# Performance work log

Hardware: AMD Instinct MI355X
Metric: run time of the kernel (lower is better)

## Reference

```python
import jax, jax.numpy as jnp
import numpy as np

N_EMBED = 1024
CUTOFFS = [20000, 60000, 180000]
N_VOCAB = 267735
BOUNDS = [0] + CUTOFFS + [N_VOCAB]            # cluster boundaries
N_EMBEDS = [1024, 256, 64, 16]                # n_embed / 4**i
N_TOK = 1024
N_CLUSTERS = len(CUTOFFS)                      # 3 tail clusters


def setup_inputs() -> dict:
    key = jax.random.key(0)
    ks = jax.random.split(key, 12)

    def w(k, shape):
        fan_in = shape[0]
        return (jax.random.normal(k, shape, jnp.float32) / np.sqrt(fan_in)).astype(jnp.float32)

    inp = {}
    inp["hidden"] = jax.random.normal(ks[0], (N_TOK, N_EMBED), jnp.float32)
    inp["target"] = jax.random.randint(ks[1], (N_TOK,), 0, N_VOCAB)
    # head: layers[0] = Linear(n_embed, cutoffs[0]); clusters = Linear(n_embed, n_clusters)
    inp["W_head"] = w(ks[2], (N_EMBED, BOUNDS[1]))
    inp["b_head"] = jnp.zeros((BOUNDS[1],), jnp.float32)
    inp["W_cluster"] = w(ks[3], (N_EMBED, N_CLUSTERS))
    inp["b_cluster"] = jnp.zeros((N_CLUSTERS,), jnp.float32)
    # tails: projections[i-1] = Linear(n_embed, n_embeds[i], bias=False); layers[i] = Linear(n_embeds[i], end-start)
    for i in range(1, N_CLUSTERS + 1):
        size = BOUNDS[i + 1] - BOUNDS[i]
        inp[f"W_proj{i}"] = w(ks[3 + 2 * i], (N_EMBED, N_EMBEDS[i]))
        inp[f"W_tail{i}"] = w(ks[4 + 2 * i], (N_EMBEDS[i], size))
        inp[f"b_tail{i}"] = jnp.zeros((size,), jnp.float32)
    return inp


def _adaptive_nll(hidden, target, W_head, b_head, W_cluster, b_cluster, tails):
    # head logits = [vocab cluster 0 | cluster logits], then log_softmax (matches torch.cat + log_softmax)
    head_logit = jnp.concatenate(
        [hidden @ W_head + b_head, hidden @ W_cluster + b_cluster], axis=1)  # [N, cut0 + n_clusters]
    head_lp = jax.nn.log_softmax(head_logit, axis=1)

    # cluster 0: logprob = head_lp[n, target]
    t0 = jnp.clip(target, 0, BOUNDS[1] - 1)
    lp0 = jnp.take_along_axis(head_lp, t0[:, None], axis=1)[:, 0]
    nll = jnp.where(target < BOUNDS[1], -lp0, jnp.zeros((), head_lp.dtype))

    # tail clusters i=1..3: logprob = head_lp[:, -i] + tail_log_softmax[n, target-start]
    for i, (Wp, Wt, bt) in enumerate(tails, start=1):
        start, end = BOUNDS[i], BOUNDS[i + 1]
        tail_lp = jax.nn.log_softmax((hidden @ Wp) @ Wt + bt, axis=1)  # [N, end-start]
        rel = jnp.clip(target - start, 0, end - start - 1)
        lp_i = head_lp[:, -i] + jnp.take_along_axis(tail_lp, rel[:, None], axis=1)[:, 0]
        in_bucket = (target >= start) & (target < end)
        nll = jnp.where(in_bucket, -lp_i, nll)
    return nll  # [N], per-token negative log-likelihood (keep_order=True semantics)


def reference(hidden, target, W_head, b_head, W_cluster, b_cluster,
              W_proj1, W_tail1, b_tail1,
              W_proj2, W_tail2, b_tail2,
              W_proj3, W_tail3, b_tail3):
    tails = [(W_proj1, W_tail1, b_tail1),
             (W_proj2, W_tail2, b_tail2),
             (W_proj3, W_tail3, b_tail3)]
    return _adaptive_nll(hidden, target, W_head, b_head, W_cluster, b_cluster, tails)
```

## Files before the change

### kernel.cpp

```cpp
#include <hip/hip_runtime.h>
#include <cstdint>
#include <cstddef>


typedef unsigned short u16;
typedef __attribute__((ext_vector_type(8))) __bf16 bf16x8;
typedef __attribute__((ext_vector_type(8))) u16 u16x8;
typedef __attribute__((ext_vector_type(4))) float f32x4;

#define AS1 __attribute__((address_space(1)))
#define AS3 __attribute__((address_space(3)))

struct MS { float m, s; };

__device__ __forceinline__ u16 f2bf(float f){
  union { float f; unsigned u; } v; v.f = f;
  unsigned r = v.u + 0x7fffu + ((v.u >> 16) & 1u);
  return (u16)(r >> 16);
}
__device__ __forceinline__ float bf2f(u16 x){
  union { unsigned u; float f; } v; v.u = ((unsigned)x) << 16;
  return v.f;
}
__device__ __forceinline__ void glds16(const void* g, void* l){
  __builtin_amdgcn_global_load_lds((AS1 unsigned*)(uintptr_t)g,
                                   (AS3 unsigned*)(unsigned)(uintptr_t)l, 16, 0, 0);
}

__global__ void k_cvt_hidden(const float* __restrict__ h, u16* __restrict__ a0,
                             int* __restrict__ cnt, int* __restrict__ trel){
  int g = blockIdx.x * 256 + threadIdx.x;
  if (g < 4096) trel[g] = -1;
  if (g < 4) cnt[g] = 0;
  int i = g * 8;
  f32x4 v0 = *(const f32x4*)(h + i);
  f32x4 v1 = *(const f32x4*)(h + i + 4);
  u16x8 o;
  o[0]=f2bf(v0.x); o[1]=f2bf(v0.y); o[2]=f2bf(v0.z); o[3]=f2bf(v0.w);
  o[4]=f2bf(v1.x); o[5]=f2bf(v1.y); o[6]=f2bf(v1.z); o[7]=f2bf(v1.w);
  *(u16x8*)(a0 + i) = o;
}

__global__ void k_compact(const int* __restrict__ tgt, int* __restrict__ cnt,
                          int* __restrict__ idx1, int* __restrict__ idx2,
                          int* __restrict__ idx3, int* __restrict__ pos,
                          int* __restrict__ tr0, int* __restrict__ tr1,
                          int* __restrict__ tr2, int* __restrict__ tr3){
  int n = blockIdx.x * 256 + threadIdx.x;
  int t = tgt[n];
  int p = 0;
  tr0[n] = (t < 20000) ? t : -1;
  if (t >= 20000){
    int b = (t < 60000) ? 0 : (t < 180000 ? 1 : 2);
    p = atomicAdd(&cnt[b], 1);
    if (b == 0){ idx1[p] = n; tr1[p] = t - 20000; }
    else if (b == 1){ idx2[p] = n; tr2[p] = t - 60000; }
    else { idx3[p] = n; tr3[p] = t - 180000; }
  }
  pos[n] = p;
}

__global__ void k_gather(const int* __restrict__ cnt,
                         const int* __restrict__ idx1, const int* __restrict__ idx2,
                         const int* __restrict__ idx3,
                         const u16* __restrict__ A1, const u16* __restrict__ A2,
                         const u16* __restrict__ A3,
                         u16* __restrict__ A1c, u16* __restrict__ A2c,
                         u16* __restrict__ A3c){
  int u = blockIdx.x * 256 + threadIdx.x;
  const u16* src; u16* dst;
  if (u < 32768){
    int r = u >> 5, c = u & 31;
    if (r >= cnt[0]) return;
    src = A1 + (size_t)idx1[r] * 256 + c * 8;
    dst = A1c + (size_t)r * 256 + c * 8;
  } else if (u < 40960){
    int v = u - 32768; int r = v >> 3, c = v & 7;
    if (r >= cnt[1]) return;
    src = A2 + (size_t)idx2[r] * 64 + c * 8;
    dst = A2c + (size_t)r * 64 + c * 8;
  } else {
    int v = u - 40960; int r = v >> 2, c = v & 3;
    if (r >= cnt[2]) return;
    src = A3 + (size_t)idx3[r] * 32 + c * 8;
    dst = A3c + (size_t)r * 32 + c * 8;
  }
  *(u16x8*)dst = *(const u16x8*)src;
}

struct TJob { const float* W; u16* BT; int K, N, Kpad, nrows, nx, base; };
struct TJobs { TJob j[8]; int nj; };

__global__ void k_transpose_multi(TJobs jobs){
  int id = blockIdx.x;
  int ji = 0;
  #pragma unroll
  for (int i = 1; i < 8; ++i)
    if (i < jobs.nj && id >= jobs.j[i].base) ji = i;
  TJob jb = jobs.j[ji];
  int local = id - jb.base;
  int bx = local % jb.nx;
  int by = local / jb.nx;

  __shared__ float t[64][65];
  const int n0 = bx * 64;
  const int k0 = by * 64;
  const bool al = (jb.N & 3) == 0;
  for (int i = threadIdx.x; i < 64*16; i += 256){
    int r = i >> 4, c4 = (i & 15) * 4;
    int k = k0 + r, n = n0 + c4;
    f32x4 v; v.x=0.f; v.y=0.f; v.z=0.f; v.w=0.f;
    if (k < jb.K){
      if (al && n + 3 < jb.N) v = *(const f32x4*)(jb.W + (size_t)k * jb.N + n);
      else { for (int q = 0; q < 4; ++q) if (n + q < jb.N) v[q] = jb.W[(size_t)k * jb.N + n + q]; }
    }
    t[r][c4] = v.x; t[r][c4+1] = v.y; t[r][c4+2] = v.z; t[r][c4+3] = v.w;
  }
  __syncthreads();
  for (int i = threadIdx.x; i < 64*8; i += 256){
    int rn = i >> 3, c8 = (i & 7) * 8;
    if (k0 + c8 < jb.Kpad && (n0 + rn) < jb.nrows){
      u16x8 o;
      #pragma unroll
      for (int q = 0; q < 8; ++q) o[q] = f2bf(t[c8 + q][rn]);
      *(u16x8*)(jb.BT + (size_t)(n0 + rn) * jb.Kpad + k0 + c8) = o;
    }
  }
}

__global__ __launch_bounds__(512)
void k_proj_gemm(const u16* __restrict__ A, const u16* __restrict__ BT,
                 const float* __restrict__ bc,
                 u16* __restrict__ A1, u16* __restrict__ A2,
                 u16* __restrict__ A3, float* __restrict__ cl)
{
  constexpr int BK = 64, K = 1024;
  __shared__ u16 As[256 * BK];
  __shared__ u16 Bs[128 * BK];
  const int tid  = threadIdx.x;
  const int lane = tid & 63, wid = tid >> 6;
  const int wm = wid & 3, wn = wid >> 2;
  const int l15 = lane & 15, l4 = lane >> 4;
  const int m0 = blockIdx.y * 256;
  const int n0 = blockIdx.x * 128;

  f32x4 acc[4][4];
  #pragma unroll
  for (int m = 0; m < 4; ++m)
    #pragma unroll
    for (int n = 0; n < 4; ++n){ acc[m][n].x=0.f; acc[m][n].y=0.f; acc[m][n].z=0.f; acc[m][n].w=0.f; }

  for (int kt = 0; kt < K / BK; ++kt){
    #pragma unroll
    for (int i = 0; i < 4; ++i){
      int c = wid * 4 + i;
      int row = c * 8 + lane / 8, kb = lane % 8;
      glds16((const char*)(A + (size_t)(m0 + row) * K + kt * BK) + kb * 16,
             (char*)As + c * 1024);
    }
    #pragma unroll
    for (int i = 0; i < 2; ++i){
      int c = wid * 2 + i;
      int row = c * 8 + lane / 8, kb = lane % 8;
      glds16((const char*)(BT + (size_t)(n0 + row) * K + kt * BK) + kb * 16,
             (char*)Bs + c * 1024);
    }
    __syncthreads();
    #pragma unroll
    for (int ks = 0; ks < 2; ++ks){
      bf16x8 af[4], bfr[4];
      #pragma unroll
      for (int m = 0; m < 4; ++m)
        af[m] = *(const bf16x8*)((const char*)As + (wm*64 + m*16 + l15) * (BK*2) + ks*64 + l4*16);
      #pragma unroll
      for (int n = 0; n < 4; ++n)
        bfr[n] = *(const bf16x8*)((const char*)Bs + (wn*64 + n*16 + l15) * (BK*2) + ks*64 + l4*16);
      #pragma unroll
      for (int m = 0; m < 4; ++m)
        #pragma unroll
        for (int n = 0; n < 4; ++n)
          acc[m][n] = __builtin_amdgcn_mfma_f32_16x16x32_bf16(af[m], bfr[n], acc[m][n], 0, 0, 0);
    }
    __syncthreads();
  }
  #pragma unroll
  for (int m = 0; m < 4; ++m)
    #pragma unroll
    for (int n = 0; n < 4; ++n)
      #pragma unroll
      for (int q = 0; q < 4; ++q){
        int c = n0 + wn*64 + n*16 + l15;
        int r = m0 + wm*64 + m*16 + l4*4 + q;
        float v = acc[m][n][q];
        if (c < 256)      A1[(size_t)r*256 + c] = f2bf(v);
        else if (c < 320) A2[(size_t)r*64 + (c-256)] = f2bf(v);
        else if (c < 336){ A3[(size_t)r*32 + (c-320)] = f2bf(v);
                           A3[(size_t)r*32 + (c-320) + 16] = 0; }
        else if (c < 339) cl[(size_t)r*3 + (c-336)] = v + bc[c-336];
      }
}

template<int BK>
__global__ __launch_bounds__(256)
void k_gemm_lse(const u16* __restrict__ A, const u16* __restrict__ BT,
                const float* __restrict__ bias, int K, int N,
                MS* __restrict__ P, int ntiles,
                const int* __restrict__ cntp, int bucket,
                const int* __restrict__ tgt_rel, const int* __restrict__ rowmap,
                float* __restrict__ tl)
{
  constexpr int BM = 128, BN = 128;
  constexpr int CH  = BK / 8;
  constexpr int LPR = CH;
  constexpr int RPC = 64 / LPR;
  constexpr int NC  = BM * BK * 2 / 1024;
  constexpr int CPW = NC / 4;
  if (cntp && (int)(blockIdx.y * BM) >= cntp[bucket]) return;
  __shared__ u16 As[BM * BK];
  __shared__ u16 Bs[BN * BK];
  __shared__ float redm[2][BM];
  __shared__ float reds[2][BM];

  const int tid  = threadIdx.x;
  const int lane = tid & 63, wid = tid >> 6;
  const int wm = wid & 1, wn = wid >> 1;
  const int l15 = lane & 15, l4 = lane >> 4;
  const int m0 = blockIdx.y * BM;
  const int n0 = blockIdx.x * BN;
  const int srow = lane / LPR;
  const int skb  = lane % LPR;

  f32x4 acc[4][4];
  #pragma unroll
  for (int m = 0; m < 4; ++m)
    #pragma unroll
    for (int n = 0; n < 4; ++n){ acc[m][n].x=0.f; acc[m][n].y=0.f; acc[m][n].z=0.f; acc[m][n].w=0.f; }

  const int ksteps = K / BK;
  for (int kt = 0; kt < ksteps; ++kt){
    #pragma unroll
    for (int i = 0; i < CPW; ++i){
      int c = wid * CPW + i;
      int row = c * RPC + srow;
      int kbs = skb ^ (row & (CH - 1));
      glds16((const char*)(A + (size_t)(m0 + row) * K + kt * BK) + kbs * 16,
             (char*)As + c * 1024);
    }
    #pragma unroll
    for (int i = 0; i < CPW; ++i){
      int c = wid * CPW + i;
      int row = c * RPC + srow;
      int kbs = skb ^ (row & (CH - 1));
      glds16((const char*)(BT + (size_t)(n0 + row) * K + kt * BK) + kbs * 16,
             (char*)Bs + c * 1024);
    }
    __syncthreads();
    #pragma unroll
    for (int ks = 0; ks < BK / 32; ++ks){
      bf16x8 af[4], bfr[4];
      #pragma unroll
      for (int m = 0; m < 4; ++m){
        int r = wm*64 + m*16 + l15;
        af[m] = *(const bf16x8*)((const char*)As + r*(BK*2) + (((ks*4 + l4) ^ (r & (CH-1))) * 16));
      }
      #pragma unroll
      for (int n = 0; n < 4; ++n){
        int r = wn*64 + n*16 + l15;
        bfr[n] = *(const bf16x8*)((const char*)Bs + r*(BK*2) + (((ks*4 + l4) ^ (r & (CH-1))) * 16));
      }
      #pragma unroll
      for (int m = 0; m < 4; ++m)
        #pragma unroll
        for (int n = 0; n < 4; ++n)
          acc[m][n] = __builtin_amdgcn_mfma_f32_16x16x32_bf16(af[m], bfr[n], acc[m][n], 0, 0, 0);
    }
    __syncthreads();
  }

  float bv[4]; bool val[4];
  #pragma unroll
  for (int n = 0; n < 4; ++n){
    int col = n0 + wn*64 + n*16 + l15;
    val[n] = col < N;
    bv[n] = val[n] ? bias[col] : 0.f;
  }
  #pragma unroll
  for (int m = 0; m < 4; ++m)
    #pragma unroll
    for (int q = 0; q < 4; ++q){
      int row = m0 + wm*64 + m*16 + l4*4 + q;
      int tr = tgt_rel[row];
      if (tr >= 0){
        #pragma unroll
        for (int n = 0; n < 4; ++n){
          int col = n0 + wn*64 + n*16 + l15;
          if (tr == col)
            tl[rowmap ? rowmap[row] : row] = acc[m][n][q] + bv[n];
        }
      }
    }
  #pragma unroll
  for (int m = 0; m < 4; ++m)
    #pragma unroll
    for (int q = 0; q < 4; ++q){
      float mx = -1e30f;
      #pragma unroll
      for (int n = 0; n < 4; ++n)
        if (val[n]) mx = fmaxf(mx, acc[m][n][q] + bv[n]);
      #pragma unroll
      for (int d = 1; d < 16; d <<= 1) mx = fmaxf(mx, __shfl_xor(mx, d));
      if (l15 == 0) redm[wn][wm*64 + m*16 + l4*4 + q] = mx;
    }
  __syncthreads();
  #pragma unroll
  for (int m = 0; m < 4; ++m)
    #pragma unroll
    for (int q = 0; q < 4; ++q){
      int lrow = wm*64 + m*16 + l4*4 + q;
      float M = fmaxf(redm[0][lrow], redm[1][lrow]);
      float s = 0.f;
      #pragma unroll
      for (int n = 0; n < 4; ++n)
        if (val[n]) s += __expf(acc[m][n][q] + bv[n] - M);
      #pragma unroll
      for (int d = 1; d < 16; d <<= 1) s += __shfl_xor(s, d);
      if (l15 == 0) reds[wn][lrow] = s;
    }
  __syncthreads();
  if (wn == 0 && l15 == 0){
    #pragma unroll
    for (int m = 0; m < 4; ++m)
      #pragma unroll
      for (int q = 0; q < 4; ++q){
        int lrow = wm*64 + m*16 + l4*4 + q;
        MS r; r.m = fmaxf(redm[0][lrow], redm[1][lrow]);
        r.s = reds[0][lrow] + reds[1][lrow];
        P[(size_t)(m0 + lrow) * ntiles + blockIdx.x] = r;
      }
  }
}

__device__ __forceinline__ void lse_merge(float& m, float& s, float m2, float s2){
  float M = fmaxf(m, m2);
  s = s * __expf(m - M) + s2 * __expf(m2 - M);
  m = M;
}

__global__ void k_finalize(const int* __restrict__ tgt, const MS* __restrict__ P,
                           const float* __restrict__ cl, const float* __restrict__ tl,
                           const int* __restrict__ pos, float* __restrict__ out)
{
  const int NT0 = 157, NT1 = 313, NT2 = 938, NT3 = 686;
  int n = blockIdx.x * 4 + (threadIdx.x >> 6);
  int lane = threadIdx.x & 63;
  int t = tgt[n];

  float m = -1e30f, s = 0.f;
  const MS* p0 = P + (size_t)n * NT0;
  for (int i = lane; i < NT0; i += 64){ MS v = p0[i]; lse_merge(m, s, v.m, v.s); }
  if (lane < 3) lse_merge(m, s, cl[n*3 + lane], 1.f);
  #pragma unroll
  for (int d = 1; d < 64; d <<= 1){
    float m2 = __shfl_xor(m, d), s2 = __shfl_xor(s, d);
    lse_merge(m, s, m2, s2);
  }
  float lse_head = m + logf(s);

  float nll;
  if (t < 20000){
    nll = lse_head - tl[n];
  } else {
    int seg, nt; size_t base;
    if      (t <  60000){ seg = 1; nt = NT1; base = (size_t)1024 * NT0; }
    else if (t < 180000){ seg = 2; nt = NT2; base = (size_t)1024 * (NT0 + NT1); }
    else                { seg = 3; nt = NT3; base = (size_t)1024 * (NT0 + NT1 + NT2); }
    float m2 = -1e30f, s2 = 0.f;
    const MS* ps = P + base + (size_t)pos[n] * nt;
    for (int i = lane; i < nt; i += 64){ MS v = ps[i]; lse_merge(m2, s2, v.m, v.s); }
    #pragma unroll
    for (int d = 1; d < 64; d <<= 1){
      float mm = __shfl_xor(m2, d), ss = __shfl_xor(s2, d);
      lse_merge(m2, s2, mm, ss);
    }
    float lse_t = m2 + logf(s2);
    nll = lse_head - cl[n*3 + (3 - seg)] + lse_t - tl[n];
  }
  if (lane == 0) out[n] = nll;
}

extern "C" void kernel_launch(void* const* d_in, const int* in_sizes, int n_in,
                              void* d_out, int out_size, void* d_ws, size_t ws_size,
                              hipStream_t stream)
{
  const float* hidden = (const float*)d_in[0];
  const int*   target = (const int*)d_in[1];
  const float* W_head = (const float*)d_in[2];
  const float* b_head = (const float*)d_in[3];
  const float* W_clu  = (const float*)d_in[4];
  const float* b_clu  = (const float*)d_in[5];
  const float* W_p1   = (const float*)d_in[6];
  const float* W_t1   = (const float*)d_in[7];
  const float* b_t1   = (const float*)d_in[8];
  const float* W_p2   = (const float*)d_in[9];
  const float* W_t2   = (const float*)d_in[10];
  const float* b_t2   = (const float*)d_in[11];
  const float* W_p3   = (const float*)d_in[12];
  const float* W_t3   = (const float*)d_in[13];
  const float* b_t3   = (const float*)d_in[14];
  float* out = (float*)d_out;

  char* ws = (char*)d_ws;
  u16*   A0  = (u16*)(ws + 0);
  u16*   A1  = (u16*)(ws + 2097152);
  u16*   A2  = (u16*)(ws + 2621440);
  u16*   A3  = (u16*)(ws + 2752512);
  float* cl  = (float*)(ws + 2818048);
  float* tl  = (float*)(ws + 2834432);
  MS*    P   = (MS*)(ws + 2838528);
  u16*   BTp = (u16*)(ws + 2838528);
  u16*   BTh = (u16*)(ws + 19992576);
  int*   cnt  = (int*)(ws + 61149184);
  int*   idx1 = (int*)(ws + 61149440);
  int*   idx2 = (int*)(ws + 61153536);
  int*   idx3 = (int*)(ws + 61157632);
  int*   pos  = (int*)(ws + 61161728);
  u16*   A1c  = (u16*)(ws + 61165824);
  u16*   A2c  = (u16*)(ws + 61690112);
  u16*   A3c  = (u16*)(ws + 61821184);
  int*   tr0  = (int*)(ws + 61886720);
  int*   tr1  = (int*)(ws + 61890816);
  int*   tr2  = (int*)(ws + 61894912);
  int*   tr3  = (int*)(ws + 61899008);
  u16*   BT1  = (u16*)(ws + 61903104);
  u16*   BT2  = (u16*)(ws + 82415872);
  u16*   BT3  = (u16*)(ws + 97784064);
  const size_t needA = 103403776;
  const bool bigws = ws_size >= needA;

  const size_t P1 = (size_t)1024 * 157;
  const size_t P2 = (size_t)1024 * (157 + 313);
  const size_t P3 = (size_t)1024 * (157 + 313 + 938);

  k_cvt_hidden<<<512, 256, 0, stream>>>(hidden, A0, cnt, tr0);
  k_compact<<<4, 256, 0, stream>>>(target, cnt, idx1, idx2, idx3, pos,
                                   tr0, tr1, tr2, tr3);

  TJobs tj{}; int nb = 0;
  auto add = [&](const float* W, u16* B, int K, int N, int Kpad, int nrows){
    int nx = (nrows + 63) / 64;
    int ny = (Kpad + 63) / 64;
    tj.j[tj.nj++] = TJob{W, B, K, N, Kpad, nrows, nx, nb};
    nb += nx * ny;
  };
  add(W_p1, BTp, 1024, 256, 1024, 256);
  add(W_p2, BTp + (size_t)256*1024, 1024, 64, 1024, 64);
  add(W_p3, BTp + (size_t)320*1024, 1024, 16, 1024, 16);
  add(W_clu, BTp + (size_t)336*1024, 1024, 3, 1024, 64);
  add(W_head, BTh, 1024, 20000, 1024, 20096);
  if (bigws){
    add(W_t1, BT1, 256, 40000, 256, 40064);
    add(W_t2, BT2, 64, 120000, 64, 120064);
    add(W_t3, BT3, 16, 87735, 32, 87808);
  }
  k_transpose_multi<<<nb, 256, 0, stream>>>(tj);

  k_proj_gemm<<<dim3(3, 4), 512, 0, stream>>>(A0, BTp, b_clu, A1, A2, A3, cl);
  k_gather<<<176, 256, 0, stream>>>(cnt, idx1, idx2, idx3, A1, A2, A3, A1c, A2c, A3c);

  k_gemm_lse<64><<<dim3(157, 8), 256, 0, stream>>>(A0, BTh, b_head, 1024, 20000,
      P, 157, nullptr, 0, tr0, nullptr, tl);

  if (bigws){
    k_gemm_lse<64><<<dim3(313, 8), 256, 0, stream>>>(A1c, BT1, b_t1, 256, 40000,
        P + P1, 313, cnt, 0, tr1, idx1, tl);
    k_gemm_lse<64><<<dim3(938, 8), 256, 0, stream>>>(A2c, BT2, b_t2, 64, 120000,
        P + P2, 938, cnt, 1, tr2, idx2, tl);
    k_gemm_lse<32><<<dim3(686, 8), 256, 0, stream>>>(A3c, BT3, b_t3, 32, 87735,
        P + P3, 686, cnt, 2, tr3, idx3, tl);
  } else {
    TJobs s1{}; s1.nj = 1; s1.j[0] = TJob{W_t1, BTh, 256, 40000, 256, 40064, 626, 0};
    k_transpose_multi<<<626*4, 256, 0, stream>>>(s1);
    k_gemm_lse<64><<<dim3(313, 8), 256, 0, stream>>>(A1c, BTh, b_t1, 256, 40000,
        P + P1, 313, cnt, 0, tr1, idx1, tl);
    TJobs s2{}; s2.nj = 1; s2.j[0] = TJob{W_t2, BTh, 64, 120000, 64, 120064, 1876, 0};
    k_transpose_multi<<<1876, 256, 0, stream>>>(s2);
    k_gemm_lse<64><<<dim3(938, 8), 256, 0, stream>>>(A2c, BTh, b_t2, 64, 120000,
        P + P2, 938, cnt, 1, tr2, idx2, tl);
    TJobs s3{}; s3.nj = 1; s3.j[0] = TJob{W_t3, BTh, 16, 87735, 32, 87808, 1372, 0};
    k_transpose_multi<<<1372, 256, 0, stream>>>(s3);
    k_gemm_lse<32><<<dim3(686, 8), 256, 0, stream>>>(A3c, BTh, b_t3, 32, 87735,
        P + P3, 686, cnt, 2, tr3, idx3, tl);
  }

  k_finalize<<<256, 256, 0, stream>>>(target, P, cl, tl, pos, out);
}
```

Before: 312.8 us.

## Add 8-wave 256x128 triple-buffered head GEMM+LSE kernel with XCD swizzle

```diff
diff --git a/kernel.cpp b/kernel.cpp
--- a/kernel.cpp
+++ b/kernel.cpp
@@ -25,6 +25,11 @@
 __device__ __forceinline__ void glds16(const void* g, void* l){
   __builtin_amdgcn_global_load_lds((AS1 unsigned*)(uintptr_t)g,
                                    (AS3 unsigned*)(unsigned)(uintptr_t)l, 16, 0, 0);
+}
+__device__ __forceinline__ void lse_merge(float& m, float& s, float m2, float s2){
+  float M = fmaxf(m, m2);
+  s = s * __expf(m - M) + s2 * __expf(m2 - M);
+  m = M;
 }
 
 __global__ void k_cvt_hidden(const float* __restrict__ h, u16* __restrict__ a0,
@@ -200,6 +205,168 @@
       }
 }
 
+template<int K, int T>
+__global__ __launch_bounds__(512)
+void k_gemm_lse8(const u16* __restrict__ A, const u16* __restrict__ BT,
+                 const float* __restrict__ bias, int N,
+                 MS* __restrict__ P, int ntiles,
+                 const int* __restrict__ tgt_rel, float* __restrict__ tl)
+{
+  __shared__ u16 sm[3 * 24576];
+  __shared__ float redm[4][256];
+  __shared__ float reds[4][256];
+
+  const int tid  = threadIdx.x;
+  const int lane = tid & 63, wid = tid >> 6;
+  const int wm = wid & 1, wn = wid >> 1;
+  const int l15 = lane & 15, l4 = lane >> 4;
+  const int srow = tid >> 3, schk = tid & 7;
+
+  const int nwg = gridDim.x;
+  int qq = nwg >> 3, rr = nwg & 7;
+  int xcd = blockIdx.x & 7, ii = blockIdx.x >> 3;
+  int swz = (xcd < rr ? xcd*(qq+1) : rr*(qq+1) + (xcd-rr)*qq) + ii;
+  const int cb = swz >> 2, rb = swz & 3;
+  const int m0 = rb * 256, n0 = cb * 128;
+
+  auto stageA = [&](int kt, int rowbase, int slot){
+    #pragma unroll
+    for (int h = 0; h < 2; ++h){
+      int r = rowbase + h*64 + srow;
+      glds16((const char*)(A + (size_t)(m0 + r)*K + kt*64) + ((schk ^ (r & 7))*16),
+             (char*)sm + slot*49152 + r*128 + schk*16);
+    }
+  };
+  auto stageB = [&](int kt, int slot){
+    #pragma unroll
+    for (int h = 0; h < 2; ++h){
+      int r = h*64 + srow;
+      glds16((const char*)(BT + (size_t)(n0 + r)*K + kt*64) + ((schk ^ (r & 7))*16),
+             (char*)sm + slot*49152 + 32768 + r*128 + schk*16);
+    }
+  };
+
+  f32x4 acc[8][2];
+  #pragma unroll
+  for (int m = 0; m < 8; ++m)
+    #pragma unroll
+    for (int n = 0; n < 2; ++n){ acc[m][n].x=0.f; acc[m][n].y=0.f; acc[m][n].z=0.f; acc[m][n].w=0.f; }
+
+  stageB(0, 0); stageA(0, 0, 0); stageA(0, 128, 0);
+  stageB(1, 1); stageA(1, 0, 1); stageA(1, 128, 1);
+  asm volatile("s_waitcnt vmcnt(6)" ::: "memory");
+  __builtin_amdgcn_s_barrier();
+  __builtin_amdgcn_sched_barrier(0);
+
+  bf16x8 bfr[2][2];
+  for (int t = 0; t < T; ++t){
+    const int slot = t % 3;
+    const char* As = (const char*)sm + slot*49152;
+    const char* Bs = As + 32768;
+    const int ps = (t + 2) % 3;
+    const bool pf = (t + 2) < T;
+    #pragma unroll
+    for (int p = 0; p < 4; ++p){
+      if (p == 0){
+        #pragma unroll
+        for (int n = 0; n < 2; ++n)
+          #pragma unroll
+          for (int ks = 0; ks < 2; ++ks){
+            int r = wn*32 + n*16 + l15;
+            bfr[n][ks] = *(const bf16x8*)(Bs + r*128 + (((ks*4 + l4) ^ (r & 7))*16));
+          }
+      }
+      bf16x8 af[2][2];
+      #pragma unroll
+      for (int mm = 0; mm < 2; ++mm)
+        #pragma unroll
+        for (int ks = 0; ks < 2; ++ks){
+          int r = (2*p + mm)*32 + wm*16 + l15;
+          af[mm][ks] = *(const bf16x8*)(As + r*128 + (((ks*4 + l4) ^ (r & 7))*16));
+        }
+      if (pf){
+        if (p == 0)      stageB(t+2, ps);
+        else if (p == 1) stageA(t+2, 0, ps);
+        else if (p == 2) stageA(t+2, 128, ps);
+      }
+      __builtin_amdgcn_s_barrier();
+      __builtin_amdgcn_s_setprio(1);
+      #pragma unroll
+      for (int mm = 0; mm < 2; ++mm)
+        #pragma unroll
+        for (int n = 0; n < 2; ++n)
+          #pragma unroll
+          for (int ks = 0; ks < 2; ++ks)
+            acc[2*p+mm][n] = __builtin_amdgcn_mfma_f32_16x16x32_bf16(
+                af[mm][ks], bfr[n][ks], acc[2*p+mm][n], 0, 0, 0);
+      __builtin_amdgcn_s_setprio(0);
+      if (p == 3){
+        if (pf) asm volatile("s_waitcnt vmcnt(6)" ::: "memory");
+        else    asm volatile("s_waitcnt vmcnt(0)" ::: "memory");
+      }
+      __builtin_amdgcn_s_barrier();
+      __builtin_amdgcn_sched_barrier(0);
+    }
+  }
+
+  float bv[2]; bool val[2];
+  #pragma unroll
+  for (int n = 0; n < 2; ++n){
+    int col = n0 + wn*32 + n*16 + l15;
+    val[n] = col < N;
+    bv[n] = val[n] ? bias[col] : 0.f;
+  }
+  #pragma unroll
+  for (int m = 0; m < 8; ++m)
+    #pragma unroll
+    for (int q = 0; q < 4; ++q){
+      int row = m0 + m*32 + wm*16 + l4*4 + q;
+      int tr = tgt_rel[row];
+      if (tr >= 0){
+        #pragma unroll
+        for (int n = 0; n < 2; ++n){
+          int col = n0 + wn*32 + n*16 + l15;
+          if (tr == col) tl[row] = acc[m][n][q] + bv[n];
+        }
+      }
+    }
+  #pragma unroll
+  for (int m = 0; m < 8; ++m)
+    #pragma unroll
+    for (int q = 0; q < 4; ++q){
+      float Ml = -1e30f, Sl = 0.f;
+      #pragma unroll
+      for (int n = 0; n < 2; ++n)
+        if (val[n]) Ml = fmaxf(Ml, acc[m][n][q] + bv[n]);
+      #pragma unroll
+      for (int n = 0; n < 2; ++n)
+        if (val[n]) Sl += __expf(acc[m][n][q] + bv[n] - Ml);
+      #pragma unroll
+      for (int d = 1; d < 16; d <<= 1){
+        float m2 = __shfl_xor(Ml, d), s2 = __shfl_xor(Sl, d);
+        lse_merge(Ml, Sl, m2, s2);
+      }
+      if (l15 == 0){
+        int lrow = m*32 + wm*16 + l4*4 + q;
+        redm[wn][lrow] = Ml; reds[wn][lrow] = Sl;
+      }
+    }
+  __syncthreads();
+  if (wn == 0 && l15 == 0){
+    #pragma unroll
+    for (int m = 0; m < 8; ++m)
+      #pragma unroll
+      for (int q = 0; q < 4; ++q){
+        int lrow = m*32 + wm*16 + l4*4 + q;
+        float M = -1e30f, S = 0.f;
+        #pragma unroll
+        for (int w = 0; w < 4; ++w) lse_merge(M, S, redm[w][lrow], reds[w][lrow]);
+        MS r; r.m = M; r.s = S;
+        P[(size_t)(m0 + lrow) * ntiles + cb] = r;
+      }
+  }
+}
+
 template<int BK>
 __global__ __launch_bounds__(256)
 void k_gemm_lse(const u16* __restrict__ A, const u16* __restrict__ BT,
@@ -303,28 +470,22 @@
   for (int m = 0; m < 4; ++m)
     #pragma unroll
     for (int q = 0; q < 4; ++q){
-      float mx = -1e30f;
+      float Ml = -1e30f, Sl = 0.f;
       #pragma unroll
       for (int n = 0; n < 4; ++n)
-        if (val[n]) mx = fmaxf(mx, acc[m][n][q] + bv[n]);
-      #pragma unroll
-      for (int d = 1; d < 16; d <<= 1) mx = fmaxf(mx, __shfl_xor(mx, d));
-      if (l15 == 0) redm[wn][wm*64 + m*16 + l4*4 + q] = mx;
-    }
-  __syncthreads();
-  #pragma unroll
-  for (int m = 0; m < 4; ++m)
-    #pragma unroll
-    for (int q = 0; q < 4; ++q){
-      int lrow = wm*64 + m*16 + l4*4 + q;
-      float M = fmaxf(redm[0][lrow], redm[1][lrow]);
-      float s = 0.f;
+        if (val[n]) Ml = fmaxf(Ml, acc[m][n][q] + bv[n]);
       #pragma unroll
       for (int n = 0; n < 4; ++n)
-        if (val[n]) s += __expf(acc[m][n][q] + bv[n] - M);
-      #pragma unroll
-      for (int d = 1; d < 16; d <<= 1) s += __shfl_xor(s, d);
-      if (l15 == 0) reds[wn][lrow] = s;
+        if (val[n]) Sl += __expf(acc[m][n][q] + bv[n] - Ml);
+      #pragma unroll
+      for (int d = 1; d < 16; d <<= 1){
+        float m2 = __shfl_xor(Ml, d), s2 = __shfl_xor(Sl, d);
+        lse_merge(Ml, Sl, m2, s2);
+      }
+      if (l15 == 0){
+        int lrow = wm*64 + m*16 + l4*4 + q;
+        redm[wn][lrow] = Ml; reds[wn][lrow] = Sl;
+      }
     }
   __syncthreads();
   if (wn == 0 && l15 == 0){
@@ -333,17 +494,12 @@
       #pragma unroll
       for (int q = 0; q < 4; ++q){
         int lrow = wm*64 + m*16 + l4*4 + q;
-        MS r; r.m = fmaxf(redm[0][lrow], redm[1][lrow]);
-        r.s = reds[0][lrow] + reds[1][lrow];
+        float M = redm[0][lrow], S = reds[0][lrow];
+        lse_merge(M, S, redm[1][lrow], reds[1][lrow]);
+        MS r; r.m = M; r.s = S;
         P[(size_t)(m0 + lrow) * ntiles + blockIdx.x] = r;
       }
   }
-}
-
-__device__ __forceinline__ void lse_merge(float& m, float& s, float m2, float s2){
-  float M = fmaxf(m, m2);
-  s = s * __expf(m - M) + s2 * __expf(m2 - M);
-  m = M;
 }
 
 __global__ void k_finalize(const int* __restrict__ tgt, const MS* __restrict__ P,
@@ -467,8 +623,8 @@
   k_proj_gemm<<<dim3(3, 4), 512, 0, stream>>>(A0, BTp, b_clu, A1, A2, A3, cl);
   k_gather<<<176, 256, 0, stream>>>(cnt, idx1, idx2, idx3, A1, A2, A3, A1c, A2c, A3c);
 
-  k_gemm_lse<64><<<dim3(157, 8), 256, 0, stream>>>(A0, BTh, b_head, 1024, 20000,
-      P, 157, nullptr, 0, tr0, nullptr, tl);
+  k_gemm_lse8<1024, 16><<<628, 512, 0, stream>>>(A0, BTh, b_head, 20000,
+      P, 157, tr0, tl);
 
   if (bigws){
     k_gemm_lse<64><<<dim3(313, 8), 256, 0, stream>>>(A1c, BT1, b_t1, 256, 40000,
```

Result: slower. 345.4 us (+10.4%).

## Merge head and tail LSE GEMMs into one launch, drop max tracking

Applied to the files above, without the earlier changes.

```diff
diff --git a/kernel.cpp b/kernel.cpp
--- a/kernel.cpp
+++ b/kernel.cpp
@@ -11,16 +11,10 @@
 #define AS1 __attribute__((address_space(1)))
 #define AS3 __attribute__((address_space(3)))
 
-struct MS { float m, s; };
-
 __device__ __forceinline__ u16 f2bf(float f){
   union { float f; unsigned u; } v; v.f = f;
   unsigned r = v.u + 0x7fffu + ((v.u >> 16) & 1u);
   return (u16)(r >> 16);
-}
-__device__ __forceinline__ float bf2f(u16 x){
-  union { unsigned u; float f; } v; v.u = ((unsigned)x) << 16;
-  return v.f;
 }
 __device__ __forceinline__ void glds16(const void* g, void* l){
   __builtin_amdgcn_global_load_lds((AS1 unsigned*)(uintptr_t)g,
@@ -80,10 +74,10 @@
     src = A2 + (size_t)idx2[r] * 64 + c * 8;
     dst = A2c + (size_t)r * 64 + c * 8;
   } else {
-    int v = u - 40960; int r = v >> 2, c = v & 3;
+    int v = u - 40960; int r = v >> 3, c = v & 7;
     if (r >= cnt[2]) return;
-    src = A3 + (size_t)idx3[r] * 32 + c * 8;
-    dst = A3c + (size_t)r * 32 + c * 8;
+    src = A3 + (size_t)idx3[r] * 64 + c * 8;
+    dst = A3c + (size_t)r * 64 + c * 8;
   }
   *(u16x8*)dst = *(const u16x8*)src;
 }
@@ -194,41 +188,45 @@
         float v = acc[m][n][q];
         if (c < 256)      A1[(size_t)r*256 + c] = f2bf(v);
         else if (c < 320) A2[(size_t)r*64 + (c-256)] = f2bf(v);
-        else if (c < 336){ A3[(size_t)r*32 + (c-320)] = f2bf(v);
-                           A3[(size_t)r*32 + (c-320) + 16] = 0; }
+        else if (c < 336){ u16* p = A3 + (size_t)r*64 + (c-320);
+                           p[0] = f2bf(v); p[16] = 0; p[32] = 0; p[48] = 0; }
         else if (c < 339) cl[(size_t)r*3 + (c-336)] = v + bc[c-336];
       }
 }
 
-template<int BK>
+struct GJob { const u16* A; const u16* BT; const float* bias; float* P;
+              const int* trel; const int* rowmap; int K, N, ntiles, cidx, base; };
+struct GJobs { GJob j[4]; int nj; };
+
 __global__ __launch_bounds__(256)
-void k_gemm_lse(const u16* __restrict__ A, const u16* __restrict__ BT,
-                const float* __restrict__ bias, int K, int N,
-                MS* __restrict__ P, int ntiles,
-                const int* __restrict__ cntp, int bucket,
-                const int* __restrict__ tgt_rel, const int* __restrict__ rowmap,
-                float* __restrict__ tl)
+void k_gemm_lse_u(GJobs jobs, const int* __restrict__ cnt, float* __restrict__ tl)
 {
-  constexpr int BM = 128, BN = 128;
-  constexpr int CH  = BK / 8;
-  constexpr int LPR = CH;
-  constexpr int RPC = 64 / LPR;
-  constexpr int NC  = BM * BK * 2 / 1024;
-  constexpr int CPW = NC / 4;
-  if (cntp && (int)(blockIdx.y * BM) >= cntp[bucket]) return;
-  __shared__ u16 As[BM * BK];
-  __shared__ u16 Bs[BN * BK];
-  __shared__ float redm[2][BM];
-  __shared__ float reds[2][BM];
+  constexpr int BK = 64, CH = 8;
+  const int nwg = gridDim.x;
+  int qd = nwg >> 3, rd = nwg & 7;
+  int xcd = blockIdx.x & 7, ii = blockIdx.x >> 3;
+  int swz = (xcd < rd ? xcd*(qd+1) : rd*(qd+1) + (xcd-rd)*qd) + ii;
+  int ji = 0;
+  #pragma unroll
+  for (int i = 1; i < 4; ++i)
+    if (i < jobs.nj && swz >= jobs.j[i].base) ji = i;
+  GJob jb = jobs.j[ji];
+  int local = swz - jb.base;
+  const int cb = local >> 3, rb = local & 7;
+  const int rows = (jb.cidx < 0) ? 1024 : cnt[jb.cidx];
+  const int m0 = rb * 128, n0 = cb * 128;
+  if (m0 >= rows) return;
+  const int K = jb.K;
+
+  __shared__ u16 As[128 * BK];
+  __shared__ u16 Bs[128 * BK];
+  __shared__ float reds[2][128];
 
   const int tid  = threadIdx.x;
   const int lane = tid & 63, wid = tid >> 6;
   const int wm = wid & 1, wn = wid >> 1;
   const int l15 = lane & 15, l4 = lane >> 4;
-  const int m0 = blockIdx.y * BM;
-  const int n0 = blockIdx.x * BN;
-  const int srow = lane / LPR;
-  const int skb  = lane % LPR;
+  const int srow = lane >> 3, skb = lane & 7;
 
   f32x4 acc[4][4];
   #pragma unroll
@@ -239,34 +237,34 @@
   const int ksteps = K / BK;
   for (int kt = 0; kt < ksteps; ++kt){
     #pragma unroll
-    for (int i = 0; i < CPW; ++i){
-      int c = wid * CPW + i;
-      int row = c * RPC + srow;
-      int kbs = skb ^ (row & (CH - 1));
-      glds16((const char*)(A + (size_t)(m0 + row) * K + kt * BK) + kbs * 16,
+    for (int i = 0; i < 4; ++i){
+      int c = wid * 4 + i;
+      int row = c * 8 + srow;
+      int kbs = skb ^ (row & 7);
+      glds16((const char*)(jb.A + (size_t)(m0 + row) * K + kt * BK) + kbs * 16,
              (char*)As + c * 1024);
     }
     #pragma unroll
-    for (int i = 0; i < CPW; ++i){
-      int c = wid * CPW + i;
-      int row = c * RPC + srow;
-      int kbs = skb ^ (row & (CH - 1));
-      glds16((const char*)(BT + (size_t)(n0 + row) * K + kt * BK) + kbs * 16,
+    for (int i = 0; i < 4; ++i){
+      int c = wid * 4 + i;
+      int row = c * 8 + srow;
+      int kbs = skb ^ (row & 7);
+      glds16((const char*)(jb.BT + (size_t)(n0 + row) * K + kt * BK) + kbs * 16,
              (char*)Bs + c * 1024);
     }
     __syncthreads();
     #pragma unroll
-    for (int ks = 0; ks < BK / 32; ++ks){
+    for (int ks = 0; ks < 2; ++ks){
       bf16x8 af[4], bfr[4];
       #pragma unroll
       for (int m = 0; m < 4; ++m){
         int r = wm*64 + m*16 + l15;
-        af[m] = *(const bf16x8*)((const char*)As + r*(BK*2) + (((ks*4 + l4) ^ (r & (CH-1))) * 16));
+        af[m] = *(const bf16x8*)((const char*)As + r*(BK*2) + (((ks*4 + l4) ^ (r & 7)) * 16));
       }
       #pragma unroll
       for (int n = 0; n < 4; ++n){
         int r = wn*64 + n*16 + l15;
-        bfr[n] = *(const bf16x8*)((const char*)Bs + r*(BK*2) + (((ks*4 + l4) ^ (r & (CH-1))) * 16));
+        bfr[n] = *(const bf16x8*)((const char*)Bs + r*(BK*2) + (((ks*4 + l4) ^ (r & 7)) * 16));
       }
       #pragma unroll
       for (int m = 0; m < 4; ++m)
@@ -281,21 +279,21 @@
   #pragma unroll
   for (int n = 0; n < 4; ++n){
     int col = n0 + wn*64 + n*16 + l15;
-    val[n] = col < N;
-    bv[n] = val[n] ? bias[col] : 0.f;
+    val[n] = col < jb.N;
+    bv[n] = val[n] ? jb.bias[col] : 0.f;
   }
   #pragma unroll
   for (int m = 0; m < 4; ++m)
     #pragma unroll
     for (int q = 0; q < 4; ++q){
       int row = m0 + wm*64 + m*16 + l4*4 + q;
-      int tr = tgt_rel[row];
+      int tr = jb.trel[row];
       if (tr >= 0){
         #pragma unroll
         for (int n = 0; n < 4; ++n){
           int col = n0 + wn*64 + n*16 + l15;
           if (tr == col)
-            tl[rowmap ? rowmap[row] : row] = acc[m][n][q] + bv[n];
+            tl[jb.rowmap ? jb.rowmap[row] : row] = acc[m][n][q] + bv[n];
         }
       }
     }
@@ -303,28 +301,13 @@
   for (int m = 0; m < 4; ++m)
     #pragma unroll
     for (int q = 0; q < 4; ++q){
-      float mx = -1e30f;
+      float Sl = 0.f;
       #pragma unroll
       for (int n = 0; n < 4; ++n)
-        if (val[n]) mx = fmaxf(mx, acc[m][n][q] + bv[n]);
-      #pragma unroll
-      for (int d = 1; d < 16; d <<= 1) mx = fmaxf(mx, __shfl_xor(mx, d));
-      if (l15 == 0) redm[wn][wm*64 + m*16 + l4*4 + q] = mx;
-    }
-  __syncthreads();
-  #pragma unroll
-  for (int m = 0; m < 4; ++m)
-    #pragma unroll
-    for (int q = 0; q < 4; ++q){
-      int lrow = wm*64 + m*16 + l4*4 + q;
-      float M = fmaxf(redm[0][lrow], redm[1][lrow]);
-      float s = 0.f;
-      #pragma unroll
-      for (int n = 0; n < 4; ++n)
-        if (val[n]) s += __expf(acc[m][n][q] + bv[n] - M);
-      #pragma unroll
-      for (int d = 1; d < 16; d <<= 1) s += __shfl_xor(s, d);
-      if (l15 == 0) reds[wn][lrow] = s;
+        if (val[n]) Sl += __expf(acc[m][n][q] + bv[n]);
+      #pragma unroll
+      for (int d = 1; d < 16; d <<= 1) Sl += __shfl_xor(Sl, d);
+      if (l15 == 0) reds[wn][wm*64 + m*16 + l4*4 + q] = Sl;
     }
   __syncthreads();
   if (wn == 0 && l15 == 0){
@@ -333,20 +316,12 @@
       #pragma unroll
       for (int q = 0; q < 4; ++q){
         int lrow = wm*64 + m*16 + l4*4 + q;
-        MS r; r.m = fmaxf(redm[0][lrow], redm[1][lrow]);
-        r.s = reds[0][lrow] + reds[1][lrow];
-        P[(size_t)(m0 + lrow) * ntiles + blockIdx.x] = r;
+        jb.P[(size_t)(m0 + lrow) * jb.ntiles + cb] = reds[0][lrow] + reds[1][lrow];
       }
   }
 }
 
-__device__ __forceinline__ void lse_merge(float& m, float& s, float m2, float s2){
-  float M = fmaxf(m, m2);
-  s = s * __expf(m - M) + s2 * __expf(m2 - M);
-  m = M;
-}
-
-__global__ void k_finalize(const int* __restrict__ tgt, const MS* __restrict__ P,
+__global__ void k_finalize(const int* __restrict__ tgt, const float* __restrict__ P,
                            const float* __restrict__ cl, const float* __restrict__ tl,
                            const int* __restrict__ pos, float* __restrict__ out)
 {
@@ -355,16 +330,13 @@
   int lane = threadIdx.x & 63;
   int t = tgt[n];
 
-  float m = -1e30f, s = 0.f;
-  const MS* p0 = P + (size_t)n * NT0;
-  for (int i = lane; i < NT0; i += 64){ MS v = p0[i]; lse_merge(m, s, v.m, v.s); }
-  if (lane < 3) lse_merge(m, s, cl[n*3 + lane], 1.f);
-  #pragma unroll
-  for (int d = 1; d < 64; d <<= 1){
-    float m2 = __shfl_xor(m, d), s2 = __shfl_xor(s, d);
-    lse_merge(m, s, m2, s2);
-  }
-  float lse_head = m + logf(s);
+  float s = 0.f;
+  const float* p0 = P + (size_t)n * NT0;
+  for (int i = lane; i < NT0; i += 64) s += p0[i];
+  if (lane < 3) s += __expf(cl[n*3 + lane]);
+  #pragma unroll
+  for (int d = 1; d < 64; d <<= 1) s += __shfl_xor(s, d);
+  float lse_head = logf(s);
 
   float nll;
   if (t < 20000){
@@ -374,15 +346,12 @@
     if      (t <  60000){ seg = 1; nt = NT1; base = (size_t)1024 * NT0; }
     else if (t < 180000){ seg = 2; nt = NT2; base = (size_t)1024 * (NT0 + NT1); }
     else                { seg = 3; nt = NT3; base = (size_t)1024 * (NT0 + NT1 + NT2); }
-    float m2 = -1e30f, s2 = 0.f;
-    const MS* ps = P + base + (size_t)pos[n] * nt;
-    for (int i = lane; i < nt; i += 64){ MS v = ps[i]; lse_merge(m2, s2, v.m, v.s); }
-    #pragma unroll
-    for (int d = 1; d < 64; d <<= 1){
-      float mm = __shfl_xor(m2, d), ss = __shfl_xor(s2, d);
-      lse_merge(m2, s2, mm, ss);
-    }
-    float lse_t = m2 + logf(s2);
+    float s2 = 0.f;
+    const float* ps = P + base + (size_t)pos[n] * nt;
+    for (int i = lane; i < nt; i += 64) s2 += ps[i];
+    #pragma unroll
+    for (int d = 1; d < 64; d <<= 1) s2 += __shfl_xor(s2, d);
+    float lse_t = logf(s2);
     nll = lse_head - cl[n*3 + (3 - seg)] + lse_t - tl[n];
   }
   if (lane == 0) out[n] = nll;
@@ -414,32 +383,33 @@
   u16*   A1  = (u16*)(ws + 2097152);
   u16*   A2  = (u16*)(ws + 2621440);
   u16*   A3  = (u16*)(ws + 2752512);
-  float* cl  = (float*)(ws + 2818048);
-  float* tl  = (float*)(ws + 2834432);
-  MS*    P   = (MS*)(ws + 2838528);
-  u16*   BTp = (u16*)(ws + 2838528);
-  u16*   BTh = (u16*)(ws + 19992576);
-  int*   cnt  = (int*)(ws + 61149184);
-  int*   idx1 = (int*)(ws + 61149440);
-  int*   idx2 = (int*)(ws + 61153536);
-  int*   idx3 = (int*)(ws + 61157632);
-  int*   pos  = (int*)(ws + 61161728);
-  u16*   A1c  = (u16*)(ws + 61165824);
-  u16*   A2c  = (u16*)(ws + 61690112);
-  u16*   A3c  = (u16*)(ws + 61821184);
-  int*   tr0  = (int*)(ws + 61886720);
-  int*   tr1  = (int*)(ws + 61890816);
-  int*   tr2  = (int*)(ws + 61894912);
-  int*   tr3  = (int*)(ws + 61899008);
-  u16*   BT1  = (u16*)(ws + 61903104);
-  u16*   BT2  = (u16*)(ws + 82415872);
-  u16*   BT3  = (u16*)(ws + 97784064);
-  const size_t needA = 103403776;
+  float* cl  = (float*)(ws + 2883584);
+  float* tl  = (float*)(ws + 2895872);
+  float* P   = (float*)(ws + 2899968);
+  u16*   BTp = (u16*)(ws + 2899968);
+  u16*   BTh = (u16*)(ws + 11476992);
+  int*   cnt  = (int*)(ws + 52633600);
+  int*   idx1 = (int*)(ws + 52633856);
+  int*   idx2 = (int*)(ws + 52637952);
+  int*   idx3 = (int*)(ws + 52642048);
+  int*   pos  = (int*)(ws + 52646144);
+  u16*   A1c  = (u16*)(ws + 52650240);
+  u16*   A2c  = (u16*)(ws + 53174528);
+  u16*   A3c  = (u16*)(ws + 53305600);
+  int*   tr0  = (int*)(ws + 53436672);
+  int*   tr1  = (int*)(ws + 53440768);
+  int*   tr2  = (int*)(ws + 53444864);
+  int*   tr3  = (int*)(ws + 53448960);
+  u16*   BT1  = (u16*)(ws + 53453056);
+  u16*   BT2  = (u16*)(ws + 73965824);
+  u16*   BT3  = (u16*)(ws + 89334016);
+  const size_t needA = 100573440;
   const bool bigws = ws_size >= needA;
 
-  const size_t P1 = (size_t)1024 * 157;
-  const size_t P2 = (size_t)1024 * (157 + 313);
-  const size_t P3 = (size_t)1024 * (157 + 313 + 938);
+  float* P0 = P;
+  float* Pp1 = P + (size_t)1024 * 157;
+  float* Pp2 = P + (size_t)1024 * (157 + 313);
+  float* Pp3 = P + (size_t)1024 * (157 + 313 + 938);
 
   k_cvt_hidden<<<512, 256, 0, stream>>>(hidden, A0, cnt, tr0);
   k_compact<<<4, 256, 0, stream>>>(target, cnt, idx1, idx2, idx3, pos,
@@ -460,36 +430,36 @@
   if (bigws){
     add(W_t1, BT1, 256, 40000, 256, 40064);
     add(W_t2, BT2, 64, 120000, 64, 120064);
-    add(W_t3, BT3, 16, 87735, 32, 87808);
+    add(W_t3, BT3, 16, 87735, 64, 87808);
   }
   k_transpose_multi<<<nb, 256, 0, stream>>>(tj);
 
   k_proj_gemm<<<dim3(3, 4), 512, 0, stream>>>(A0, BTp, b_clu, A1, A2, A3, cl);
-  k_gather<<<176, 256, 0, stream>>>(cnt, idx1, idx2, idx3, A1, A2, A3, A1c, A2c, A3c);
-
-  k_gemm_lse<64><<<dim3(157, 8), 256, 0, stream>>>(A0, BTh, b_head, 1024, 20000,
-      P, 157, nullptr, 0, tr0, nullptr, tl);
-
+  k_gather<<<192, 256, 0, stream>>>(cnt, idx1, idx2, idx3, A1, A2, A3, A1c, A2c, A3c);
+
+  GJob jh{A0,  BTh, b_head, P0,  tr0, nullptr, 1024, 20000, 157, -1, 0};
+  GJob j1{A1c, BT1, b_t1,   Pp1, tr1, idx1,    256,  40000, 313,  0, 1256};
+  GJob j2{A2c, BT2, b_t2,   Pp2, tr2, idx2,    64,  120000, 938,  1, 3760};
+  GJob j3{A3c, BT3, b_t3,   Pp3, tr3, idx3,    64,   87735, 686,  2, 11264};
   if (bigws){
-    k_gemm_lse<64><<<dim3(313, 8), 256, 0, stream>>>(A1c, BT1, b_t1, 256, 40000,
-        P + P1, 313, cnt, 0, tr1, idx1, tl);
-    k_gemm_lse<64><<<dim3(938, 8), 256, 0, stream>>>(A2c, BT2, b_t2, 64, 120000,
-        P + P2, 938, cnt, 1, tr2, idx2, tl);
-    k_gemm_lse<32><<<dim3(686, 8), 256, 0, stream>>>(A3c, BT3, b_t3, 32, 87735,
-        P + P3, 686, cnt, 2, tr3, idx3, tl);
+    GJobs gj{}; gj.nj = 4;
+    gj.j[0] = jh; gj.j[1] = j1; gj.j[2] = j2; gj.j[3] = j3;
+    k_gemm_lse_u<<<16752, 256, 0, stream>>>(gj, cnt, tl);
   } else {
+    GJobs g0{}; g0.nj = 1; g0.j[0] = jh;
+    k_gemm_lse_u<<<1256, 256, 0, stream>>>(g0, cnt, tl);
     TJobs s1{}; s1.nj = 1; s1.j[0] = TJob{W_t1, BTh, 256, 40000, 256, 40064, 626, 0};
     k_transpose_multi<<<626*4, 256, 0, stream>>>(s1);
-    k_gemm_lse<64><<<dim3(313, 8), 256, 0, stream>>>(A1c, BTh, b_t1, 256, 40000,
-        P + P1, 313, cnt, 0, tr1, idx1, tl);
+    GJobs g1{}; g1.nj = 1; g1.j[0] = j1; g1.j[0].BT = BTh; g1.j[0].base = 0;
+    k_gemm_lse_u<<<2504, 256, 0, stream>>>(g1, cnt, tl);
     TJobs s2{}; s2.nj = 1; s2.j[0] = TJob{W_t2, BTh, 64, 120000, 64, 120064, 1876, 0};
     k_transpose_multi<<<1876, 256, 0, stream>>>(s2);
-    k_gemm_lse<64><<<dim3(938, 8), 256, 0, stream>>>(A2c, BTh, b_t2, 64, 120000,
-        P + P2, 938, cnt, 1, tr2, idx2, tl);
-    TJobs s3{}; s3.nj = 1; s3.j[0] = TJob{W_t3, BTh, 16, 87735, 32, 87808, 1372, 0};
+    GJobs g2{}; g2.nj = 1; g2.j[0] = j2; g2.j[0].BT = BTh; g2.j[0].base = 0;
+    k_gemm_lse_u<<<7504, 256, 0, stream>>>(g2, cnt, tl);
+    TJobs s3{}; s3.nj = 1; s3.j[0] = TJob{W_t3, BTh, 16, 87735, 64, 87808, 1372, 0};
     k_transpose_multi<<<1372, 256, 0, stream>>>(s3);
-    k_gemm_lse<32><<<dim3(686, 8), 256, 0, stream>>>(A3c, BTh, b_t3, 32, 87735,
-        P + P3, 686, cnt, 2, tr3, idx3, tl);
+    GJobs g3{}; g3.nj = 1; g3.j[0] = j3; g3.j[0].BT = BTh; g3.j[0].base = 0;
+    k_gemm_lse_u<<<5488, 256, 0, stream>>>(g3, cnt, tl);
   }
 
   k_finalize<<<256, 256, 0, stream>>>(target, P, cl, tl, pos, out);
```

After: 534.6 us. 1.71x slower.
